# Kernel tuning notes

Hardware: AMD Instinct MI355X
Metric: run time of the kernel (lower is better)

Reference implementation:

```python
import jax, jax.numpy as jnp
import numpy as np

N = 100_000      # nodes
E = 3_200_000    # edges (avg degree 32)
IN = 128         # input feature dim
H1, C1 = 8, 8    # layer-1 heads, channels per head (concat -> 64)
OUT = 2          # output classes (layer-2: 1 head, mean/no-concat)
NEG = 0.2        # LeakyReLU negative slope (PyG default)


def setup_inputs() -> dict:
    key = jax.random.key(0)
    ks = jax.random.split(key, 11)
    s1 = 1.0 / np.sqrt(IN)
    s2 = 1.0 / np.sqrt(H1 * C1)
    return {
        "x": jax.random.normal(ks[0], (N, IN), jnp.float32),
        "edge_index": jax.random.randint(ks[1], (2, E), 0, N, dtype=jnp.int32),
        "edge_attr": jax.random.normal(ks[2], (E, 1), jnp.float32),
        "W1": jax.random.normal(ks[3], (IN, H1 * C1), jnp.float32) * s1,
        "a1_src": jax.random.normal(ks[4], (H1, C1), jnp.float32) * s1,
        "a1_dst": jax.random.normal(ks[5], (H1, C1), jnp.float32) * s1,
        "b1": jnp.zeros((H1 * C1,), jnp.float32),
        "W2": jax.random.normal(ks[6], (H1 * C1, OUT), jnp.float32) * s2,
        "a2_src": jax.random.normal(ks[7], (1, OUT), jnp.float32) * s2,
        "a2_dst": jax.random.normal(ks[8], (1, OUT), jnp.float32) * s2,
        "b2": jnp.zeros((OUT,), jnp.float32),
    }


def gat_conv(x, W, a_src, a_dst, b, src, dst, heads, ch, concat):
    """PyG GATConv: per-head linear, per-edge LeakyReLU attention, segment softmax over dst."""
    n = x.shape[0]
    h = (x @ W).reshape(n, heads, ch)                 # [N, H, C]
    al_src = jnp.sum(h * a_src, axis=-1)              # [N, H]
    al_dst = jnp.sum(h * a_dst, axis=-1)              # [N, H]
    e = al_src[src] + al_dst[dst]                     # [Etot, H]
    e = jnp.where(e > 0, e, NEG * e)                  # LeakyReLU
    m = jax.lax.stop_gradient(jax.ops.segment_max(e, dst, num_segments=n))
    ex = jnp.exp(e - m[dst])
    den = jax.ops.segment_sum(ex, dst, num_segments=n)
    alpha = ex / den[dst]                             # segment softmax
    out = jax.ops.segment_sum(alpha[:, :, None] * h[src], dst, num_segments=n)  # [N, H, C]
    out = out.reshape(n, heads * ch) if concat else out.mean(axis=1)
    return out + b


def reference(x, edge_index, edge_attr, W1, a1_src, a1_dst, b1, W2, a2_src, a2_dst, b2):
    # add_self_loops=True (PyG default)
    loops = jnp.arange(x.shape[0], dtype=edge_index.dtype)
    src = jnp.concatenate([edge_index[0], loops])
    dst = jnp.concatenate([edge_index[1], loops])
    h = gat_conv(x, W1, a1_src, a1_dst, b1, src, dst, H1, C1, True)
    h = jax.nn.elu(h)
    return gat_conv(h, W2, a2_src, a2_dst, b2, src, dst, 1, OUT, False)
```

## Files before the change

kernel.cpp:

```cpp
#include <hip/hip_runtime.h>
#include <math.h>

#define NNODES 100000
#define NEDGES 3200000
#define ETOT   (NEDGES + NNODES)
#define IN_DIM 128
#define NH1    8
#define NC1    8
#define HC     64
#define OUTC   2
#define NEGSL  0.2f
#define L2E    1.44269504f

#define NBUCK 391
#define EPB   8192
#define NBLK  391
#define TOTC  (NBUCK * NBLK)


__global__ __launch_bounds__(256) void histA(const int* __restrict__ ei,
                                             int* __restrict__ carr) {
    __shared__ int lh[NBUCK];
    int tid = threadIdx.x;
    for (int i = tid; i < NBUCK; i += 256) lh[i] = 0;
    __syncthreads();
    const int* dptr = ei + NEDGES;
    int base = blockIdx.x * EPB;
#pragma unroll
    for (int i = 0; i < EPB / 1024; i++) {
        int idx = base + i * 1024 + tid * 4;
        if (idx < NEDGES) {
            int4 d4 = *(const int4*)&dptr[idx];
            atomicAdd(&lh[d4.x >> 8], 1);
            atomicAdd(&lh[d4.y >> 8], 1);
            atomicAdd(&lh[d4.z >> 8], 1);
            atomicAdd(&lh[d4.w >> 8], 1);
        }
    }
    __syncthreads();
    for (int i = tid; i < NBUCK; i += 256)
        carr[i * NBLK + blockIdx.x] = lh[i];
}

__global__ __launch_bounds__(256) void scanA(int* __restrict__ carr,
                                             int* __restrict__ bsums) {
    int gid = blockIdx.x * 256 + threadIdx.x;
    int v = (gid < TOTC) ? carr[gid] : 0;
    int lane = threadIdx.x & 63, w = threadIdx.x >> 6;
    int x = v;
    for (int off = 1; off < 64; off <<= 1) {
        int y = __shfl_up(x, off, 64);
        if (lane >= off) x += y;
    }
    __shared__ int wt[4];
    if (lane == 63) wt[w] = x;
    __syncthreads();
    int add = 0;
    for (int i = 0; i < w; i++) add += wt[i];
    int incl = x + add;
    if (gid < TOTC) carr[gid] = incl - v;
    if (threadIdx.x == 255) bsums[blockIdx.x] = incl;
}

__global__ __launch_bounds__(1024) void scanB(int* __restrict__ bsums, int nb) {
    int tid = threadIdx.x;
    int v = (tid < nb) ? bsums[tid] : 0;
    int lane = tid & 63, w = tid >> 6;
    int x = v;
    for (int off = 1; off < 64; off <<= 1) {
        int y = __shfl_up(x, off, 64);
        if (lane >= off) x += y;
    }
    __shared__ int wt[16];
    if (lane == 63) wt[w] = x;
    __syncthreads();
    int add = 0;
    for (int i = 0; i < w; i++) add += wt[i];
    if (tid < nb) bsums[tid] = x + add - v;
}

__global__ __launch_bounds__(256) void scanC(int* __restrict__ carr,
                                             const int* __restrict__ bsums) {
    int gid = blockIdx.x * 256 + threadIdx.x;
    if (gid < TOTC) carr[gid] += bsums[gid >> 8];
}

__global__ __launch_bounds__(256) void scatC(const int* __restrict__ ei,
                                             const int* __restrict__ soff,
                                             int* __restrict__ ebuf) {
    __shared__ int soffL[NBUCK];
    __shared__ int lh[NBUCK];
    int tid = threadIdx.x;
    for (int i = tid; i < NBUCK; i += 256) {
        soffL[i] = soff[i * NBLK + blockIdx.x];
        lh[i] = 0;
    }
    __syncthreads();
    int base = blockIdx.x * EPB;
#pragma unroll
    for (int i = 0; i < EPB / 1024; i++) {
        int idx = base + i * 1024 + tid * 4;
        if (idx < NEDGES) {
            int4 s4 = *(const int4*)&ei[idx];
            int4 d4 = *(const int4*)&ei[NEDGES + idx];
            int b0 = d4.x >> 8, b1 = d4.y >> 8, b2 = d4.z >> 8, b3 = d4.w >> 8;
            int r0 = atomicAdd(&lh[b0], 1);
            int r1 = atomicAdd(&lh[b1], 1);
            int r2 = atomicAdd(&lh[b2], 1);
            int r3 = atomicAdd(&lh[b3], 1);
            ebuf[soffL[b0] + r0] = s4.x | ((d4.x & 255) << 17);
            ebuf[soffL[b1] + r1] = s4.y | ((d4.y & 255) << 17);
            ebuf[soffL[b2] + r2] = s4.z | ((d4.z & 255) << 17);
            ebuf[soffL[b3] + r3] = s4.w | ((d4.w & 255) << 17);
        }
    }
}

__global__ __launch_bounds__(256) void buildD(const int* __restrict__ soff,
                                              const int* __restrict__ ebuf,
                                              int* __restrict__ rowoff,
                                              int* __restrict__ srcs) {
    int b = blockIdx.x, tid = threadIdx.x;
    int nb = min(256, NNODES - b * 256);
    int ebeg = soff[b * NBLK];
    int eend = (b == NBUCK - 1) ? NEDGES : soff[(b + 1) * NBLK];
    __shared__ int cnt2[256];
    __shared__ int rowL[256];
    __shared__ int wsum[4];
    cnt2[tid] = 0;
    __syncthreads();
    for (int e = ebeg + tid; e < eend; e += 256)
        atomicAdd(&cnt2[(ebuf[e] >> 17) & 255], 1);
    __syncthreads();
    int v = (tid < nb) ? cnt2[tid] + 1 : 0;
    int lane = tid & 63, w = tid >> 6;
    int x = v;
    for (int off = 1; off < 64; off <<= 1) {
        int y = __shfl_up(x, off, 64);
        if (lane >= off) x += y;
    }
    if (lane == 63) wsum[w] = x;
    __syncthreads();
    int add = 0;
    for (int i = 0; i < w; i++) add += wsum[i];
    int fbase = ebeg + b * 256;
    int row = fbase + x + add - v;
    if (tid < nb) {
        rowL[tid] = row;
        int gnode = b * 256 + tid;
        rowoff[gnode] = row;
        srcs[row + cnt2[tid]] = gnode;
        if (gnode == NNODES - 1) rowoff[NNODES] = ETOT;
    }
    __syncthreads();
    cnt2[tid] = 0;
    __syncthreads();
    for (int e = ebeg + tid; e < eend; e += 256) {
        int wv = ebuf[e];
        int dl = (wv >> 17) & 255;
        int r = atomicAdd(&cnt2[dl], 1);
        srcs[rowL[dl] + r] = wv & 0x1FFFF;
    }
}


__global__ __launch_bounds__(256) void gemm1(const float* __restrict__ x,
                                             const float* __restrict__ W1,
                                             const float* __restrict__ a1s,
                                             const float* __restrict__ a1d,
                                             float* __restrict__ h1,
                                             float2* __restrict__ alE,
                                             float* __restrict__ al1d) {
    __shared__ float sW[IN_DIM * HC];
    int tid = threadIdx.x;
    const float4* W4 = (const float4*)W1;
    float4* sW4 = (float4*)sW;
#pragma unroll
    for (int i = 0; i < 8; i++)
        sW4[tid + i * 256] = W4[tid + i * 256];
    __syncthreads();

    int w = __builtin_amdgcn_readfirstlane(tid >> 6);
    int lane = tid & 63;
    int node0 = blockIdx.x * 16 + w * 4;
    const float* xr = x + (size_t)node0 * IN_DIM;

    float acc0 = 0.f, acc1 = 0.f, acc2 = 0.f, acc3 = 0.f;
#pragma unroll 8
    for (int k = 0; k < IN_DIM; k++) {
        float wv = sW[k * HC + lane];
        acc0 = fmaf(xr[k], wv, acc0);
        acc1 = fmaf(xr[IN_DIM + k], wv, acc1);
        acc2 = fmaf(xr[2 * IN_DIM + k], wv, acc2);
        acc3 = fmaf(xr[3 * IN_DIM + k], wv, acc3);
    }

    float accs[4] = {acc0, acc1, acc2, acc3};
    int head = lane >> 3, c = lane & 7;
    float as = a1s[head * NC1 + c], adv = a1d[head * NC1 + c];
#pragma unroll
    for (int n = 0; n < 4; n++) {
        int node = node0 + n;
        h1[node * HC + lane] = accs[n];
        float ps = accs[n] * as;
        float pd = accs[n] * adv;
        for (int off = 1; off < 8; off <<= 1) {
            ps += __shfl_xor(ps, off, 64);
            pd += __shfl_xor(pd, off, 64);
        }
        if (c == 0) {
            alE[node * NH1 + head] = make_float2(exp2f(ps * L2E),
                                                 exp2f(ps * (NEGSL * L2E)));
            al1d[node * NH1 + head] = pd;
        }
    }
}


__global__ __launch_bounds__(256) void agg1(const float* __restrict__ h1,
                                            const float2* __restrict__ alE,
                                            const float* __restrict__ al1d,
                                            const float* __restrict__ b1,
                                            const float* __restrict__ W2,
                                            const float* __restrict__ a2s,
                                            const float* __restrict__ a2d,
                                            const int* __restrict__ rowoff,
                                            const int* __restrict__ srcs,
                                            float* __restrict__ h2,
                                            float2* __restrict__ al2E,
                                            float* __restrict__ al2d) {
    int w = threadIdx.x >> 6, lane = threadIdx.x & 63;
    int node = blockIdx.x * 4 + w;
    if (node >= NNODES) return;
    int h = lane >> 3;
    float ald = al1d[node * NH1 + h];
    float E1d = exp2f(ald * L2E);
    float E2d = exp2f(ald * (NEGSL * L2E));
    int beg = __builtin_amdgcn_readfirstlane(rowoff[node]);
    int end = __builtin_amdgcn_readfirstlane(rowoff[node + 1]);

    float den = 0.f, acc = 0.f, denB = 0.f, accB = 0.f;
    int i = beg;
    for (; i + 4 <= end; i += 4) {
        int s0 = __builtin_amdgcn_readfirstlane(srcs[i]);
        int s1 = __builtin_amdgcn_readfirstlane(srcs[i + 1]);
        int s2 = __builtin_amdgcn_readfirstlane(srcs[i + 2]);
        int s3 = __builtin_amdgcn_readfirstlane(srcs[i + 3]);
        float2 e0 = alE[s0 * NH1 + h];
        float2 e1 = alE[s1 * NH1 + h];
        float2 e2 = alE[s2 * NH1 + h];
        float2 e3 = alE[s3 * NH1 + h];
        float hv0 = h1[s0 * HC + lane];
        float hv1 = h1[s1 * HC + lane];
        float hv2 = h1[s2 * HC + lane];
        float hv3 = h1[s3 * HC + lane];
        float p0 = fmaxf(e0.x * E1d, e0.y * E2d);
        float p1 = fmaxf(e1.x * E1d, e1.y * E2d);
        float p2 = fmaxf(e2.x * E1d, e2.y * E2d);
        float p3 = fmaxf(e3.x * E1d, e3.y * E2d);
        den  += p0;  acc  = fmaf(p0, hv0, acc);
        denB += p1;  accB = fmaf(p1, hv1, accB);
        den  += p2;  acc  = fmaf(p2, hv2, acc);
        denB += p3;  accB = fmaf(p3, hv3, accB);
    }
    for (; i < end; ++i) {
        int s0 = __builtin_amdgcn_readfirstlane(srcs[i]);
        float2 e0 = alE[s0 * NH1 + h];
        float hv0 = h1[s0 * HC + lane];
        float p0 = fmaxf(e0.x * E1d, e0.y * E2d);
        den += p0; acc = fmaf(p0, hv0, acc);
    }
    den += denB; acc += accB;

    float o = acc / den + b1[lane];
    o = (o > 0.f) ? o : expm1f(o);
    float p0 = o * W2[lane * OUTC + 0];
    float p1 = o * W2[lane * OUTC + 1];
    for (int off = 1; off < 64; off <<= 1) {
        p0 += __shfl_xor(p0, off, 64);
        p1 += __shfl_xor(p1, off, 64);
    }
    if (lane == 0) {
        h2[node * 2 + 0] = p0;
        h2[node * 2 + 1] = p1;
        float l2s = p0 * a2s[0] + p1 * a2s[1];
        float l2d = p0 * a2d[0] + p1 * a2d[1];
        al2E[node] = make_float2(exp2f(l2s * L2E), exp2f(l2s * (NEGSL * L2E)));
        al2d[node] = l2d;
    }
}


__global__ __launch_bounds__(256) void agg2(const float* __restrict__ h2,
                                            const float2* __restrict__ al2E,
                                            const float* __restrict__ al2d,
                                            const float* __restrict__ b2,
                                            const int* __restrict__ rowoff,
                                            const int* __restrict__ srcs,
                                            float* __restrict__ out) {
    int w = threadIdx.x >> 6, lane = threadIdx.x & 63;
    int n = blockIdx.x * 4 + w;
    if (n >= NNODES) return;
    float ald = al2d[n];
    float E1d = exp2f(ald * L2E);
    float E2d = exp2f(ald * (NEGSL * L2E));
    int beg = rowoff[n], end = rowoff[n + 1];
    float den = 0.f, a0 = 0.f, a1 = 0.f;
    for (int idx = beg + lane; idx < end; idx += 64) {
        int s = srcs[idx];
        float2 es = al2E[s];
        float2 q = *(const float2*)&h2[s * 2];
        float p = fmaxf(es.x * E1d, es.y * E2d);
        den += p;
        a0 = fmaf(p, q.x, a0);
        a1 = fmaf(p, q.y, a1);
    }
    for (int off = 1; off < 64; off <<= 1) {
        den += __shfl_xor(den, off, 64);
        a0  += __shfl_xor(a0, off, 64);
        a1  += __shfl_xor(a1, off, 64);
    }
    if (lane == 0) {
        out[n * 2 + 0] = a0 / den + b2[0];
        out[n * 2 + 1] = a1 / den + b2[1];
    }
}


extern "C" void kernel_launch(void* const* d_in, const int* in_sizes, int n_in,
                              void* d_out, int out_size, void* d_ws, size_t ws_size,
                              hipStream_t stream) {
    const float* x   = (const float*)d_in[0];
    const int*   ei  = (const int*)  d_in[1];
    const float* W1  = (const float*)d_in[3];
    const float* a1s = (const float*)d_in[4];
    const float* a1d = (const float*)d_in[5];
    const float* b1  = (const float*)d_in[6];
    const float* W2  = (const float*)d_in[7];
    const float* a2s = (const float*)d_in[8];
    const float* a2d = (const float*)d_in[9];
    const float* b2  = (const float*)d_in[10];
    float* out = (float*)d_out;

    float* fws    = (float*)d_ws;
    float* h1     = fws;
    int*   ebuf   = (int*)fws;
    int*   carr   = ebuf + NEDGES;
    int*   bsums  = carr + TOTC;
    float2* alE   = (float2*)(h1 + (size_t)NNODES * HC);
    float* al1d_  = (float*)(alE + (size_t)NNODES * NH1);
    float* h2     = al1d_ + (size_t)NNODES * NH1;
    float2* al2E  = (float2*)(h2 + (size_t)NNODES * 2);
    float* al2d_  = (float*)(al2E + NNODES);
    int* rowoff   = (int*)(al2d_ + NNODES);
    int* srcs     = rowoff + NNODES + 1;

    const int NB_SC  = (TOTC + 255) / 256;
    const int NB_N4  = (NNODES + 3) / 4;
    const int NB_G   = NNODES / 16;

    histA<<<NBLK, 256, 0, stream>>>(ei, carr);
    scanA<<<NB_SC, 256, 0, stream>>>(carr, bsums);
    scanB<<<1, 1024, 0, stream>>>(bsums, NB_SC);
    scanC<<<NB_SC, 256, 0, stream>>>(carr, bsums);
    scatC<<<NBLK, 256, 0, stream>>>(ei, carr, ebuf);
    buildD<<<NBUCK, 256, 0, stream>>>(carr, ebuf, rowoff, srcs);

    gemm1<<<NB_G, 256, 0, stream>>>(x, W1, a1s, a1d, h1, alE, al1d_);

    agg1<<<NB_N4, 256, 0, stream>>>(h1, alE, al1d_, b1, W2, a2s, a2d,
                                    rowoff, srcs, h2, al2E, al2d_);

    agg2<<<NB_N4, 256, 0, stream>>>(h2, al2E, al2d_, b2, rowoff, srcs, out);
}
```

Baseline: 301.6 us.

## Store layer-1 features as bf16, pack layer-2 node data, shrink sort blocks

Layer-1 projected features are rounded to bf16 on write and expanded back to fp32 during the edge gather. This halves the bytes fetched per neighbour in the dominant aggregation kernel. Layer-2 per-node values (exp terms plus the two projected features) are packed into one float4 so agg2 does a single gather per edge. The bucket sort now uses 2048 edges per block across 1563 blocks, with scanB processing four partial sums per thread to cover the larger count. The bf16 rounding adds precision loss in the aggregation.

```diff
diff --git a/kernel.cpp b/kernel.cpp
--- a/kernel.cpp
+++ b/kernel.cpp
@@ -13,8 +13,8 @@
 #define L2E    1.44269504f
 
 #define NBUCK 391
-#define EPB   8192
-#define NBLK  391
+#define EPB   2048
+#define NBLK  1563
 #define TOTC  (NBUCK * NBLK)
 
 
@@ -64,9 +64,15 @@
 
 __global__ __launch_bounds__(1024) void scanB(int* __restrict__ bsums, int nb) {
     int tid = threadIdx.x;
-    int v = (tid < nb) ? bsums[tid] : 0;
+    int base = tid * 4;
+    int v[4]; int tot = 0;
+#pragma unroll
+    for (int j = 0; j < 4; j++) {
+        v[j] = (base + j < nb) ? bsums[base + j] : 0;
+        tot += v[j];
+    }
     int lane = tid & 63, w = tid >> 6;
-    int x = v;
+    int x = tot;
     for (int off = 1; off < 64; off <<= 1) {
         int y = __shfl_up(x, off, 64);
         if (lane >= off) x += y;
@@ -76,7 +82,12 @@
     __syncthreads();
     int add = 0;
     for (int i = 0; i < w; i++) add += wt[i];
-    if (tid < nb) bsums[tid] = x + add - v;
+    int pre = x + add - tot;
+#pragma unroll
+    for (int j = 0; j < 4; j++) {
+        if (base + j < nb) bsums[base + j] = pre;
+        pre += v[j];
+    }
 }
 
 __global__ __launch_bounds__(256) void scanC(int* __restrict__ carr,
@@ -168,7 +179,7 @@
                                              const float* __restrict__ W1,
                                              const float* __restrict__ a1s,
                                              const float* __restrict__ a1d,
-                                             float* __restrict__ h1,
+                                             unsigned short* __restrict__ h1b,
                                              float2* __restrict__ alE,
                                              float* __restrict__ al1d) {
     __shared__ float sW[IN_DIM * HC];
@@ -201,7 +212,9 @@
 #pragma unroll
     for (int n = 0; n < 4; n++) {
         int node = node0 + n;
-        h1[node * HC + lane] = accs[n];
+        unsigned int u = __float_as_uint(accs[n]);
+        h1b[node * HC + lane] =
+            (unsigned short)((u + 0x7FFF + ((u >> 16) & 1)) >> 16);
         float ps = accs[n] * as;
         float pd = accs[n] * adv;
         for (int off = 1; off < 8; off <<= 1) {
@@ -217,7 +230,7 @@
 }
 
 
-__global__ __launch_bounds__(256) void agg1(const float* __restrict__ h1,
+__global__ __launch_bounds__(256) void agg1(const unsigned short* __restrict__ h1b,
                                             const float2* __restrict__ alE,
                                             const float* __restrict__ al1d,
                                             const float* __restrict__ b1,
@@ -226,8 +239,7 @@
                                             const float* __restrict__ a2d,
                                             const int* __restrict__ rowoff,
                                             const int* __restrict__ srcs,
-                                            float* __restrict__ h2,
-                                            float2* __restrict__ al2E,
+                                            float4* __restrict__ nd2,
                                             float* __restrict__ al2d) {
     int w = threadIdx.x >> 6, lane = threadIdx.x & 63;
     int node = blockIdx.x * 4 + w;
@@ -250,10 +262,10 @@
         float2 e1 = alE[s1 * NH1 + h];
         float2 e2 = alE[s2 * NH1 + h];
         float2 e3 = alE[s3 * NH1 + h];
-        float hv0 = h1[s0 * HC + lane];
-        float hv1 = h1[s1 * HC + lane];
-        float hv2 = h1[s2 * HC + lane];
-        float hv3 = h1[s3 * HC + lane];
+        float hv0 = __uint_as_float((unsigned int)h1b[s0 * HC + lane] << 16);
+        float hv1 = __uint_as_float((unsigned int)h1b[s1 * HC + lane] << 16);
+        float hv2 = __uint_as_float((unsigned int)h1b[s2 * HC + lane] << 16);
+        float hv3 = __uint_as_float((unsigned int)h1b[s3 * HC + lane] << 16);
         float p0 = fmaxf(e0.x * E1d, e0.y * E2d);
         float p1 = fmaxf(e1.x * E1d, e1.y * E2d);
         float p2 = fmaxf(e2.x * E1d, e2.y * E2d);
@@ -266,7 +278,7 @@
     for (; i < end; ++i) {
         int s0 = __builtin_amdgcn_readfirstlane(srcs[i]);
         float2 e0 = alE[s0 * NH1 + h];
-        float hv0 = h1[s0 * HC + lane];
+        float hv0 = __uint_as_float((unsigned int)h1b[s0 * HC + lane] << 16);
         float p0 = fmaxf(e0.x * E1d, e0.y * E2d);
         den += p0; acc = fmaf(p0, hv0, acc);
     }
@@ -281,18 +293,16 @@
         p1 += __shfl_xor(p1, off, 64);
     }
     if (lane == 0) {
-        h2[node * 2 + 0] = p0;
-        h2[node * 2 + 1] = p1;
         float l2s = p0 * a2s[0] + p1 * a2s[1];
         float l2d = p0 * a2d[0] + p1 * a2d[1];
-        al2E[node] = make_float2(exp2f(l2s * L2E), exp2f(l2s * (NEGSL * L2E)));
+        nd2[node] = make_float4(exp2f(l2s * L2E), exp2f(l2s * (NEGSL * L2E)),
+                                p0, p1);
         al2d[node] = l2d;
     }
 }
 
 
-__global__ __launch_bounds__(256) void agg2(const float* __restrict__ h2,
-                                            const float2* __restrict__ al2E,
+__global__ __launch_bounds__(256) void agg2(const float4* __restrict__ nd2,
                                             const float* __restrict__ al2d,
                                             const float* __restrict__ b2,
                                             const int* __restrict__ rowoff,
@@ -308,12 +318,11 @@
     float den = 0.f, a0 = 0.f, a1 = 0.f;
     for (int idx = beg + lane; idx < end; idx += 64) {
         int s = srcs[idx];
-        float2 es = al2E[s];
-        float2 q = *(const float2*)&h2[s * 2];
-        float p = fmaxf(es.x * E1d, es.y * E2d);
+        float4 nd = nd2[s];
+        float p = fmaxf(nd.x * E1d, nd.y * E2d);
         den += p;
-        a0 = fmaf(p, q.x, a0);
-        a1 = fmaf(p, q.y, a1);
+        a0 = fmaf(p, nd.z, a0);
+        a1 = fmaf(p, nd.w, a1);
     }
     for (int off = 1; off < 64; off <<= 1) {
         den += __shfl_xor(den, off, 64);
@@ -342,18 +351,17 @@
     const float* b2  = (const float*)d_in[10];
     float* out = (float*)d_out;
 
-    float* fws    = (float*)d_ws;
-    float* h1     = fws;
-    int*   ebuf   = (int*)fws;
-    int*   carr   = ebuf + NEDGES;
-    int*   bsums  = carr + TOTC;
-    float2* alE   = (float2*)(h1 + (size_t)NNODES * HC);
+    char* ws = (char*)d_ws;
+    unsigned short* h1b = (unsigned short*)ws;
+    float2* alE   = (float2*)(ws + (size_t)NNODES * HC * 2);
     float* al1d_  = (float*)(alE + (size_t)NNODES * NH1);
-    float* h2     = al1d_ + (size_t)NNODES * NH1;
-    float2* al2E  = (float2*)(h2 + (size_t)NNODES * 2);
-    float* al2d_  = (float*)(al2E + NNODES);
+    float4* nd2   = (float4*)(al1d_ + (size_t)NNODES * NH1);
+    float* al2d_  = (float*)(nd2 + NNODES);
     int* rowoff   = (int*)(al2d_ + NNODES);
     int* srcs     = rowoff + NNODES + 1;
+    int* ebuf     = (int*)ws;
+    int* carr     = ebuf + NEDGES;
+    int* bsums    = carr + TOTC;
 
     const int NB_SC  = (TOTC + 255) / 256;
     const int NB_N4  = (NNODES + 3) / 4;
@@ -366,10 +374,10 @@
     scatC<<<NBLK, 256, 0, stream>>>(ei, carr, ebuf);
     buildD<<<NBUCK, 256, 0, stream>>>(carr, ebuf, rowoff, srcs);
 
-    gemm1<<<NB_G, 256, 0, stream>>>(x, W1, a1s, a1d, h1, alE, al1d_);
-
-    agg1<<<NB_N4, 256, 0, stream>>>(h1, alE, al1d_, b1, W2, a2s, a2d,
-                                    rowoff, srcs, h2, al2E, al2d_);
-
-    agg2<<<NB_N4, 256, 0, stream>>>(h2, al2E, al2d_, b2, rowoff, srcs, out);
-}
+    gemm1<<<NB_G, 256, 0, stream>>>(x, W1, a1s, a1d, h1b, alE, al1d_);
+
+    agg1<<<NB_N4, 256, 0, stream>>>(h1b, alE, al1d_, b1, W2, a2s, a2d,
+                                    rowoff, srcs, nd2, al2d_);
+
+    agg2<<<NB_N4, 256, 0, stream>>>(nd2, al2d_, b2, rowoff, srcs, out);
+}
```

Result: faster. 282.2 us (-6.4%).
